# Kernel optimization log

Measured on AMD Instinct MI355X. Metric: run time of the kernel, lower is better.

The kernel has to match this reference:

```python
import math
import jax, jax.numpy as jnp
import numpy as np

B, L, D = 2, 2048, 768
H, DK = 12, 64
NUM_BUCKETS, MAX_DIST = 32, 128


def _relative_position_bucket(rel, bidirectional=True, num_buckets=32, max_distance=128):
    # rel: [Lq, Lk] int32, rel = k_pos - q_pos
    ret = jnp.zeros_like(rel)
    n = -rel
    if bidirectional:
        num_buckets //= 2
        ret = ret + (n < 0).astype(jnp.int32) * num_buckets
        n = jnp.abs(n)
    else:
        n = jnp.maximum(n, 0)
    max_exact = num_buckets // 2
    is_small = n < max_exact
    # safe log: avoid log(0); masked by where(is_small, ...)
    n_safe = jnp.maximum(n, 1).astype(jnp.float32)
    val_if_large = max_exact + (
        jnp.log(n_safe / max_exact) / math.log(max_distance / max_exact) * (num_buckets - max_exact)
    ).astype(jnp.int32)
    val_if_large = jnp.minimum(val_if_large, num_buckets - 1)
    return ret + jnp.where(is_small, n, val_if_large)


def setup_inputs() -> dict:
    key = jax.random.key(0)
    ks = jax.random.split(key, 7)
    s = 1.0 / math.sqrt(D)
    return {
        "query": jax.random.normal(ks[0], (B, L, D), jnp.float32),
        "key_value": jax.random.normal(ks[1], (B, L, D), jnp.float32),
        "key_padding_mask": jnp.ones((B, L), jnp.int32),
        "Wq": jax.random.normal(ks[2], (D, H * DK), jnp.float32) * s,
        "Wk": jax.random.normal(ks[3], (D, H * DK), jnp.float32) * s,
        "Wv": jax.random.normal(ks[4], (D, H * DK), jnp.float32) * s,
        "Wo": jax.random.normal(ks[5], (H * DK, D), jnp.float32) * s,
        "rel_emb": jax.random.normal(ks[6], (NUM_BUCKETS, H), jnp.float32),
    }


def reference(query, key_value, key_padding_mask, Wq, Wk, Wv, Wo, rel_emb):
    Bq, Lq, _ = query.shape
    Lk = key_value.shape[1]
    scale = DK ** (-0.5)

    Q = (query @ Wq).reshape(Bq, Lq, H, DK).transpose(0, 2, 1, 3)      # [B,H,Lq,DK]
    K = (key_value @ Wk).reshape(Bq, Lk, H, DK).transpose(0, 2, 1, 3)  # [B,H,Lk,DK]
    V = (key_value @ Wv).reshape(Bq, Lk, H, DK).transpose(0, 2, 1, 3)

    scores = jnp.einsum("bhqd,bhkd->bhqk", Q, K) * scale               # [B,H,Lq,Lk]

    # T5 relative position bias (bidirectional, causal_mask=False)
    rel = jnp.arange(Lk, dtype=jnp.int32)[None, :] - jnp.arange(Lq, dtype=jnp.int32)[:, None]
    buckets = _relative_position_bucket(rel, True, NUM_BUCKETS, MAX_DIST)  # [Lq,Lk]
    bias = rel_emb[buckets]                                             # [Lq,Lk,H]
    scores = scores + bias.transpose(2, 0, 1)[None]                     # [1,H,Lq,Lk]

    pad = (key_padding_mask == 0)[:, None, None, :]                     # [B,1,1,Lk]
    scores = jnp.where(pad, -jnp.inf, scores)

    attn = jax.nn.softmax(scores.astype(jnp.float32), axis=-1).astype(Q.dtype)
    out = jnp.einsum("bhqk,bhkd->bhqd", attn, V)                        # [B,H,Lq,DK]
    out = out.transpose(0, 2, 1, 3).reshape(Bq, Lq, H * DK)
    return out @ Wo
```

## Files before the change

kernel.cpp:

```cpp
#include <hip/hip_runtime.h>
#include <stdint.h>

typedef __attribute__((ext_vector_type(8))) short bf16x8;
typedef __attribute__((ext_vector_type(4))) float f32x4;
typedef __attribute__((ext_vector_type(4))) unsigned int u32x4;

#define NB 2
#define NL 2048
#define ND 768
#define NH 12
#define NDK 64
#define NM 4096
#define LOG2E 1.4426950408889634f

template<int N> struct IC { static constexpr int v = N; };

__device__ __forceinline__ unsigned short f2bf(float f) {
  unsigned u = __builtin_bit_cast(unsigned, f);
  u += 0x7FFFu + ((u >> 16) & 1u);
  return (unsigned short)(u >> 16);
}

__device__ __forceinline__ float fexp2(float x) {
  float r;
  asm("v_exp_f32 %0, %1" : "=v"(r) : "v"(x));
  return r;
}

__device__ __forceinline__ float xmax32(float x) { return fmaxf(x, __shfl_xor(x, 32)); }
__device__ __forceinline__ float xsum32(float x) { return x + __shfl_xor(x, 32); }

__device__ __forceinline__ void gl_lds16(const unsigned short* g, unsigned short* l) {
  __builtin_amdgcn_global_load_lds((const __attribute__((address_space(1))) void*)g,
                                   (__attribute__((address_space(3))) void*)l, 16, 0, 0);
}

__global__ __launch_bounds__(256) void k_prep(const float* __restrict__ query,
                                              const float* __restrict__ keyval,
                                              const float* __restrict__ Wq,
                                              const float* __restrict__ Wk,
                                              const float* __restrict__ Wv,
                                              const float* __restrict__ Wo,
                                              const float* __restrict__ rel_emb,
                                              const int* __restrict__ mask,
                                              unsigned short* __restrict__ q_bf,
                                              unsigned short* __restrict__ kv_bf,
                                              unsigned short* __restrict__ Wq_t,
                                              unsigned short* __restrict__ Wk_t,
                                              unsigned short* __restrict__ Wv_t,
                                              unsigned short* __restrict__ Wo_t,
                                              float* __restrict__ bias_tab,
                                              float* __restrict__ maskadd,
                                              int* __restrict__ maskall) {
  __shared__ float shbuf[32 * 33];
  int blk = blockIdx.x, tid = threadIdx.x;
  if (blk < 6144) {
    int y = blk / 3072;
    int i = (blk - y * 3072) * 256 + tid;
    const float* src = y ? keyval : query;
    unsigned short* dst = y ? kv_bf : q_bf;
    float4 v = ((const float4*)src)[i];
    ushort4 o;
    o.x = f2bf(v.x); o.y = f2bf(v.y); o.z = f2bf(v.z); o.w = f2bf(v.w);
    ((ushort4*)dst)[i] = o;
  } else if (blk < 8448) {
    int rel = blk - 6144;
    int z = rel / 576, r2 = rel - z * 576;
    int bx = (r2 % 24) * 32, by = (r2 / 24) * 32;
    const float* w = (z == 0) ? Wq : (z == 1) ? Wk : (z == 2) ? Wv : Wo;
    unsigned short* o = (z == 0) ? Wq_t : (z == 1) ? Wk_t : (z == 2) ? Wv_t : Wo_t;
    float scale = (z == 0) ? 0.125f * LOG2E : 1.0f;
    int tx = tid & 31, ty = tid >> 5;
    float (*t)[33] = (float(*)[33])shbuf;
    for (int r = 0; r < 32; r += 8)
      t[ty + r][tx] = w[(by + ty + r) * ND + bx + tx];
    __syncthreads();
    for (int r = 0; r < 32; r += 8)
      o[(bx + ty + r) * ND + by + tx] = f2bf(t[tx][ty + r] * scale);
  } else if (blk < 8640) {
    int idx = (blk - 8448) * 256 + tid;
    if (idx >= 4095 * NH) return;
    int h = idx % NH;
    int di = idx / NH;
    int rel = di - 2047;
    int n = -rel;
    int ret = 0;
    if (n < 0) { ret = 16; n = -n; }
    int b;
    if (n < 8) {
      b = ret + n;
    } else {
      int v = (n >= 91) ? 7 : (n >= 64) ? 6 : (n >= 46) ? 5 : (n >= 32) ? 4
            : (n >= 23) ? 3 : (n >= 16) ? 2 : (n >= 12) ? 1 : 0;
      b = ret + 8 + v;
    }
    bias_tab[h * 4095 + di] = rel_emb[b * NH + h] * LOG2E;
  } else {
    int b = blk - 8640;
    int* red = (int*)shbuf;
    int acc = 1;
    for (int i = tid; i < NL; i += 256) {
      int m = mask[b * NL + i];
      maskadd[b * NL + i] = m ? 0.0f : -1e30f;
      acc &= (m != 0) ? 1 : 0;
    }
    red[tid] = acc;
    __syncthreads();
    for (int s2 = 128; s2 > 0; s2 >>= 1) {
      if (tid < s2) red[tid] &= red[tid + s2];
      __syncthreads();
    }
    if (tid == 0) maskall[b] = red[0];
  }
}

__global__ __launch_bounds__(256) void k_gemm_qkv(const unsigned short* __restrict__ q_bf,
                                                  const unsigned short* __restrict__ kv_bf,
                                                  const unsigned short* __restrict__ Wt,
                                                  unsigned short* __restrict__ Qb,
                                                  unsigned short* __restrict__ Kb,
                                                  unsigned short* __restrict__ Vt) {
  __shared__ unsigned short S[14336];
  unsigned short* As = S;
  unsigned short* Bs = S + 8192;
  int tid = threadIdx.x;
  int wave = tid >> 6, lane = tid & 63;
  int lr = lane & 15, lg = lane >> 4;
  int m0 = blockIdx.x * 128;
  int z = blockIdx.y >> 3;
  int nc0 = (blockIdx.y & 7) * 96;
  const unsigned short* A  = (z == 0) ? q_bf : kv_bf;
  const unsigned short* Bt = Wt + (size_t)blockIdx.y * 96 * ND;
  int wm = (wave >> 1) * 64, wn = (wave & 1) * 48;
  int srow = tid >> 3, spc = tid & 7;
  int sg = spc ^ (srow & 7);
  const unsigned short* Ag = A  + (size_t)(m0 + srow) * ND + sg * 8;
  const unsigned short* Bg = Bt + (size_t)srow * ND + sg * 8;
  f32x4 acc[4][3] = {};
  for (int t = 0; t < ND / 64; ++t) {
    int k0 = t * 64;
#pragma unroll
    for (int s = 0; s < 4; ++s)
      gl_lds16(Ag + (size_t)(s * 32) * ND + k0, &As[s * 2048 + tid * 8]);
#pragma unroll
    for (int s = 0; s < 3; ++s)
      gl_lds16(Bg + (size_t)(s * 32) * ND + k0, &Bs[s * 2048 + tid * 8]);
    __syncthreads();
#pragma unroll
    for (int ks = 0; ks < 2; ++ks) {
      bf16x8 af[4], bfr[3];
#pragma unroll
      for (int i = 0; i < 4; ++i) {
        int ar = wm + i * 16 + lr;
        af[i] = *(const bf16x8*)&As[ar * 64 + (((ks * 4 + lg) ^ (ar & 7)) * 8)];
      }
#pragma unroll
      for (int i = 0; i < 3; ++i) {
        int br = wn + i * 16 + lr;
        bfr[i] = *(const bf16x8*)&Bs[br * 64 + (((ks * 4 + lg) ^ (br & 7)) * 8)];
      }
#pragma unroll
      for (int mi = 0; mi < 4; ++mi)
#pragma unroll
        for (int ni = 0; ni < 3; ++ni)
          acc[mi][ni] = __builtin_amdgcn_mfma_f32_16x16x32_bf16(af[mi], bfr[ni], acc[mi][ni], 0, 0, 0);
    }
    __syncthreads();
  }
  if (z == 2) {
    unsigned short* T = S;
#pragma unroll
    for (int mi = 0; mi < 4; ++mi)
#pragma unroll
      for (int ni = 0; ni < 3; ++ni) {
        int col  = wn + ni * 16 + lr;
        int rowb = wm + mi * 16 + lg * 4;
        ushort4 v4;
        v4.x = f2bf(acc[mi][ni][0]);
        v4.y = f2bf(acc[mi][ni][1]);
        v4.z = f2bf(acc[mi][ni][2]);
        v4.w = f2bf(acc[mi][ni][3]);
        int addr = col * 128 + (((rowb >> 3) ^ (col & 7)) * 8) + (rowb & 7);
        *(ushort4*)&T[addr] = v4;
      }
    __syncthreads();
    int bb = m0 >> 11;
    unsigned short* vdst = Vt + (((size_t)bb * ND + nc0) << 11) + (m0 & 2047);
#pragma unroll
    for (int pass = 0; pass < 6; ++pass) {
      int col = (tid >> 4) + pass * 16;
      int cc = tid & 15;
      u32x4 val = *(const u32x4*)&T[col * 128 + ((cc ^ (col & 7)) * 8)];
      *(u32x4*)&vdst[((size_t)col << 11) + cc * 8] = val;
    }
  } else {
#pragma unroll
    for (int mi = 0; mi < 4; ++mi)
#pragma unroll
      for (int ni = 0; ni < 3; ++ni)
#pragma unroll
        for (int r = 0; r < 4; ++r) {
          int row = m0 + wm + mi * 16 + lg * 4 + r;
          int col = nc0 + wn + ni * 16 + lr;
          unsigned short v = f2bf(acc[mi][ni][r]);
          if (z == 0) Qb[(size_t)row * ND + col] = v;
          else        Kb[(size_t)row * ND + col] = v;
        }
  }
}

__global__ __launch_bounds__(256) void k_gemm(const unsigned short* __restrict__ A,
                                              const unsigned short* __restrict__ Bt,
                                              float* __restrict__ Cout,
                                              int Msz, int Nsz, int Ksz) {
  __shared__ unsigned short As[4096];
  __shared__ unsigned short Bs[4096];
  int tid = threadIdx.x;
  int wave = tid >> 6, lane = tid & 63;
  int lr = lane & 15, lg = lane >> 4;
  int m0 = blockIdx.x * 64, n0 = blockIdx.y * 64;
  int wm = (wave >> 1) * 32, wn = (wave & 1) * 32;
  int srow = tid >> 3, spc = tid & 7;
  int sg = spc ^ (srow & 7);
  const unsigned short* Ag = A  + (size_t)(m0 + srow) * Ksz + sg * 8;
  const unsigned short* Bg = Bt + (size_t)(n0 + srow) * Ksz + sg * 8;
  f32x4 acc[2][2] = {};
  for (int t = 0; t < Ksz / 64; ++t) {
    int k0 = t * 64;
#pragma unroll
    for (int s = 0; s < 2; ++s) {
      gl_lds16(Ag + (size_t)(s * 32) * Ksz + k0, &As[s * 2048 + tid * 8]);
      gl_lds16(Bg + (size_t)(s * 32) * Ksz + k0, &Bs[s * 2048 + tid * 8]);
    }
    __syncthreads();
#pragma unroll
    for (int ks = 0; ks < 2; ++ks) {
      bf16x8 af[2], bfr[2];
#pragma unroll
      for (int i = 0; i < 2; ++i) {
        int ar = wm + i * 16 + lr;
        af[i] = *(const bf16x8*)&As[ar * 64 + (((ks * 4 + lg) ^ (ar & 7)) * 8)];
        int br = wn + i * 16 + lr;
        bfr[i] = *(const bf16x8*)&Bs[br * 64 + (((ks * 4 + lg) ^ (br & 7)) * 8)];
      }
#pragma unroll
      for (int mi = 0; mi < 2; ++mi)
#pragma unroll
        for (int ni = 0; ni < 2; ++ni)
          acc[mi][ni] = __builtin_amdgcn_mfma_f32_16x16x32_bf16(af[mi], bfr[ni], acc[mi][ni], 0, 0, 0);
    }
    __syncthreads();
  }
#pragma unroll
  for (int mi = 0; mi < 2; ++mi)
#pragma unroll
    for (int ni = 0; ni < 2; ++ni)
#pragma unroll
      for (int r = 0; r < 4; ++r) {
        int row = m0 + wm + mi * 16 + lg * 4 + r;
        int col = n0 + wn + ni * 16 + lr;
        Cout[(size_t)row * Nsz + col] = acc[mi][ni][r];
      }
}

__global__ __launch_bounds__(256, 3) void k_attn(const unsigned short* __restrict__ Qb,
                                                 const unsigned short* __restrict__ Kb,
                                                 const unsigned short* __restrict__ Vt,
                                                 const float* __restrict__ bias_tab,
                                                 const float* __restrict__ maskadd,
                                                 const int* __restrict__ maskall,
                                                 unsigned short* __restrict__ Ob) {
  __shared__ unsigned short Ks[3][4096];
  __shared__ unsigned short Vs[3][4096];
  __shared__ float biasw[384];
  int flat = blockIdx.x;
  int nf = (flat & 7) * 96 + (flat >> 3);
  int qt = nf & 31, bh = nf >> 5;
  int b = bh / NH, h = bh % NH;
  int tid = threadIdx.x, wave = tid >> 6, lane = tid & 63;
  int lr = lane & 15, lg = lane >> 4;
  int q0 = qt * 64;
  for (int i = tid; i < 383; i += 256) biasw[i] = bias_tab[h * 4095 + 1856 + i];
  float cFlo = bias_tab[h * 4095];
  float cFhi = bias_tab[h * 4095 + 4094];
  const unsigned short* Kbase = Kb + (size_t)(b * NL) * ND + h * NDK;
  const unsigned short* Vbase = Vt + (size_t)(b * NH + h) * NDK * NL;
  int srow = tid >> 3, spc = tid & 7;
  int sg = spc ^ (srow & 7);
  int l0 = (srow >> 4) * 32 + ((srow >> 2) & 3) * 8 + (srow & 3);
  const unsigned short* Kg0 = Kbase + (size_t)l0 * ND + sg * 8;
  const unsigned short* Kg1 = Kbase + (size_t)(l0 + 4) * ND + sg * 8;
  const unsigned short* Vg0 = Vbase + (size_t)srow * NL + sg * 8;
  const unsigned short* Vg1 = Vbase + (size_t)(32 + srow) * NL + sg * 8;
  bf16x8 aq[2];
  int qw = q0 + wave * 16;
#pragma unroll
  for (int ks = 0; ks < 2; ++ks)
    aq[ks] = *(const bf16x8*)&Qb[(size_t)(b * NL + qw + lr) * ND + h * NDK + ks * 32 + lg * 8];
  const float* cbase = maskadd + b * NL;
  int nomask = __builtin_amdgcn_readfirstlane(maskall[b]);
  f32x4 accO[4] = {};
  float mst = -1e30f, lstl = 0.f;
  int bconst = lg * 8 - wave * 16 - lr + 191 - q0;
  int src0 = (lane & 48) | ((lane >> 2) & 12);
  gl_lds16(Kg0, &Ks[0][tid * 8]);
  gl_lds16(Kg1, &Ks[0][2048 + tid * 8]);
  gl_lds16(Vg0, &Vs[0][tid * 8]);
  gl_lds16(Vg1, &Vs[0][2048 + tid * 8]);
  {
    size_t kok = (size_t)64 * ND, kov = 64;
    gl_lds16(Kg0 + kok, &Ks[1][tid * 8]);
    gl_lds16(Kg1 + kok, &Ks[1][2048 + tid * 8]);
    gl_lds16(Vg0 + kov, &Vs[1][tid * 8]);
    gl_lds16(Vg1 + kov, &Vs[1][2048 + tid * 8]);
  }
  asm volatile("s_waitcnt vmcnt(4) lgkmcnt(0)" ::: "memory");
  __builtin_amdgcn_s_barrier();
  const unsigned short* sk0 = Kg0 + (size_t)2 * 64 * ND;
  const unsigned short* sk1 = Kg1 + (size_t)2 * 64 * ND;
  const unsigned short* sv0 = Vg0 + 2 * 64;
  const unsigned short* sv1 = Vg1 + 2 * 64;

  auto body = [&](int kt_, auto CURc, auto PFc) {
    constexpr int CUR = decltype(CURc)::v;
    constexpr int PF  = decltype(PFc)::v;
    constexpr int ST  = (CUR + 2) % 3;
    float4 cv[2][2];
    if (!nomask) {
#pragma unroll
      for (int hf = 0; hf < 2; ++hf)
#pragma unroll
        for (int qd = 0; qd < 2; ++qd)
          cv[hf][qd] = *(const float4*)&cbase[kt_ * 64 + hf * 32 + lg * 8 + qd * 4];
    }
    if (PF) {
      gl_lds16(sk0, &Ks[ST][tid * 8]);
      gl_lds16(sk1, &Ks[ST][2048 + tid * 8]);
      gl_lds16(sv0, &Vs[ST][tid * 8]);
      gl_lds16(sv1, &Vs[ST][2048 + tid * 8]);
      sk0 += 64 * ND; sk1 += 64 * ND; sv0 += 64; sv1 += 64;
    }
    int kt64 = kt_ * 64;
    bool farlo = (kt64 + 63 < q0 - 90), farhi = (kt64 > q0 + 153);
    float ctile = farlo ? cFlo : (farhi ? cFhi : 0.0f);
    f32x4 s[4];
    __builtin_amdgcn_s_setprio(1);
    if (nomask && (farlo || farhi)) {
      const f32x4 z = {0.f, 0.f, 0.f, 0.f};
#pragma unroll
      for (int ni = 0; ni < 4; ++ni) {
        int kr = ni * 16 + lr;
        bf16x8 bk0 = *(const bf16x8*)&Ks[CUR][kr * 64 + ((lg ^ (lr & 7)) * 8)];
        bf16x8 bk1 = *(const bf16x8*)&Ks[CUR][kr * 64 + (((4 + lg) ^ (lr & 7)) * 8)];
        s[ni] = __builtin_amdgcn_mfma_f32_16x16x32_bf16(bk0, aq[0], z, 0, 0, 0);
        s[ni] = __builtin_amdgcn_mfma_f32_16x16x32_bf16(bk1, aq[1], s[ni], 0, 0, 0);
      }
    } else {
      if (farlo || farhi) {
#pragma unroll
        for (int ni = 0; ni < 4; ++ni)
#pragma unroll
          for (int r = 0; r < 4; ++r) s[ni][r] = 0.f;
      } else {
#pragma unroll
        for (int ni = 0; ni < 4; ++ni)
#pragma unroll
          for (int r = 0; r < 4; ++r)
            s[ni][r] = biasw[kt64 + (ni & 1) * 32 + (ni >> 1) * 4 + r + bconst];
      }
      if (!nomask) {
#pragma unroll
        for (int ni = 0; ni < 4; ++ni)
#pragma unroll
          for (int r = 0; r < 4; ++r)
            s[ni][r] += ((const float*)&cv[ni & 1][ni >> 1])[r];
      }
#pragma unroll
      for (int ni = 0; ni < 4; ++ni) {
        int kr = ni * 16 + lr;
        bf16x8 bk0 = *(const bf16x8*)&Ks[CUR][kr * 64 + ((lg ^ (lr & 7)) * 8)];
        bf16x8 bk1 = *(const bf16x8*)&Ks[CUR][kr * 64 + (((4 + lg) ^ (lr & 7)) * 8)];
        s[ni] = __builtin_amdgcn_mfma_f32_16x16x32_bf16(bk0, aq[0], s[ni], 0, 0, 0);
        s[ni] = __builtin_amdgcn_mfma_f32_16x16x32_bf16(bk1, aq[1], s[ni], 0, 0, 0);
      }
    }
    __builtin_amdgcn_s_setprio(0);
    f32x4 t0, t1;
#pragma unroll
    for (int r = 0; r < 4; ++r) t0[r] = fmaxf(s[0][r], s[1][r]);
#pragma unroll
    for (int r = 0; r < 4; ++r) t1[r] = fmaxf(s[2][r], s[3][r]);
#pragma unroll
    for (int r = 0; r < 4; ++r) t0[r] = fmaxf(t0[r], t1[r]);
    float lm = fmaxf(fmaxf(t0[0], t0[1]), fmaxf(t0[2], t0[3]));
    if (!__all(lm + ctile - mst <= 8.0f)) {
      float pmax = fmaxf(lm, __shfl_xor(lm, 16));
      pmax = xmax32(pmax);
      float pm2 = pmax + ctile;
      float mnew = fmaxf(mst, pm2);
      float sc = fexp2(mst - mnew);
      float scB[4];
#pragma unroll
      for (int r = 0; r < 4; ++r) scB[r] = __shfl(sc, src0 | r);
#pragma unroll
      for (int ni = 0; ni < 4; ++ni)
#pragma unroll
        for (int r = 0; r < 4; ++r) accO[ni][r] *= scB[r];
      lstl *= sc;
      mst = mnew;
    }
    float msub = mst - ctile;
#pragma unroll
    for (int ni = 0; ni < 4; ++ni)
#pragma unroll
      for (int r = 0; r < 4; ++r) s[ni][r] = fexp2(s[ni][r] - msub);
    {
      f32x4 ta = s[0] + s[1];
      f32x4 tb = s[2] + s[3];
      ta = ta + tb;
      lstl += (ta[0] + ta[1]) + (ta[2] + ta[3]);
    }
    unsigned pw[8];
#pragma unroll
    for (int ni = 0; ni < 4; ++ni) {
      unsigned a, c;
      asm("v_cvt_pk_bf16_f32 %0, %1, %2" : "=v"(a) : "v"(s[ni][0]), "v"(s[ni][1]));
      asm("v_cvt_pk_bf16_f32 %0, %1, %2" : "=v"(c) : "v"(s[ni][2]), "v"(s[ni][3]));
      pw[ni * 2] = a; pw[ni * 2 + 1] = c;
    }
    u32x4 apw0 = {pw[0], pw[1], pw[4], pw[5]};
    u32x4 apw1 = {pw[2], pw[3], pw[6], pw[7]};
    bf16x8 ap0 = __builtin_bit_cast(bf16x8, apw0);
    bf16x8 ap1 = __builtin_bit_cast(bf16x8, apw1);
    __builtin_amdgcn_s_setprio(1);
#pragma unroll
    for (int ni = 0; ni < 4; ++ni) {
      int vr = ni * 16 + lr;
      bf16x8 bv0 = *(const bf16x8*)&Vs[CUR][vr * 64 + ((lg ^ (lr & 7)) * 8)];
      bf16x8 bv1 = *(const bf16x8*)&Vs[CUR][vr * 64 + (((4 + lg) ^ (lr & 7)) * 8)];
      accO[ni] = __builtin_amdgcn_mfma_f32_16x16x32_bf16(ap0, bv0, accO[ni], 0, 0, 0);
      accO[ni] = __builtin_amdgcn_mfma_f32_16x16x32_bf16(ap1, bv1, accO[ni], 0, 0, 0);
    }
    __builtin_amdgcn_s_setprio(0);
    if (PF) asm volatile("s_waitcnt vmcnt(4)" ::: "memory");
    else    asm volatile("s_waitcnt vmcnt(0)" ::: "memory");
    __builtin_amdgcn_s_barrier();
  };

  for (int kt = 0; kt < 30; kt += 3) {
    body(kt,     IC<0>{}, IC<1>{});
    body(kt + 1, IC<1>{}, IC<1>{});
    body(kt + 2, IC<2>{}, IC<1>{});
  }
  body(30, IC<0>{}, IC<0>{});
  body(31, IC<1>{}, IC<0>{});

  float lst = lstl + __shfl_xor(lstl, 16);
  lst = xsum32(lst);
  float linv = 1.0f / lst;
  float lB[4];
#pragma unroll
  for (int r = 0; r < 4; ++r) lB[r] = __shfl(linv, src0 | r);
#pragma unroll
  for (int ni = 0; ni < 4; ++ni)
#pragma unroll
    for (int r = 0; r < 4; ++r) {
      int qg = qw + lg * 4 + r;
      int col = h * NDK + ni * 16 + lr;
      Ob[(size_t)(b * NL + qg) * ND + col] = f2bf(accO[ni][r] * lB[r]);
    }
}

extern "C" void kernel_launch(void* const* d_in, const int* in_sizes, int n_in,
                              void* d_out, int out_size, void* d_ws, size_t ws_size,
                              hipStream_t stream) {
  const float* query  = (const float*)d_in[0];
  const float* keyval = (const float*)d_in[1];
  const int*   mask   = (const int*)d_in[2];
  const float* Wq     = (const float*)d_in[3];
  const float* Wk     = (const float*)d_in[4];
  const float* Wv     = (const float*)d_in[5];
  const float* Wo     = (const float*)d_in[6];
  const float* rel    = (const float*)d_in[7];

  char* ws = (char*)d_ws;
  unsigned short* q_bf  = (unsigned short*)(ws);
  unsigned short* kv_bf = (unsigned short*)(ws + 6291456);
  unsigned short* Wq_t  = (unsigned short*)(ws + 12582912);
  unsigned short* Wk_t  = (unsigned short*)(ws + 13762560);
  unsigned short* Wv_t  = (unsigned short*)(ws + 14942208);
  unsigned short* Wo_t  = (unsigned short*)(ws + 16121856);
  unsigned short* Qb    = (unsigned short*)(ws + 17301504);
  unsigned short* Kb    = (unsigned short*)(ws + 23592960);
  unsigned short* Vt    = (unsigned short*)(ws + 29884416);
  unsigned short* Ob    = (unsigned short*)(ws + 36175872);
  float* bias_tab       = (float*)(ws + 42467328);
  float* maskadd        = (float*)(ws + 42663936);
  int*   maskall        = (int*)(ws + 42680320);

  k_prep<<<dim3(8642), dim3(256), 0, stream>>>(query, keyval, Wq, Wk, Wv, Wo, rel, mask,
                                               q_bf, kv_bf, Wq_t, Wk_t, Wv_t, Wo_t,
                                               bias_tab, maskadd, maskall);
  k_gemm_qkv<<<dim3(32, 24), dim3(256), 0, stream>>>(q_bf, kv_bf, Wq_t, Qb, Kb, Vt);
  k_attn<<<dim3(768), dim3(256), 0, stream>>>(Qb, Kb, Vt, bias_tab, maskadd, maskall, Ob);
  k_gemm<<<dim3(64, 12), dim3(256), 0, stream>>>(Ob, Wo_t, (float*)d_out, NM, ND, ND);
}
```

Baseline: 93.31 us.

## Remap GEMM block indices for XCD locality and double-buffer output projection

Result: no change. 93.18 us (-0.1%).

```diff
diff --git a/kernel.cpp b/kernel.cpp
--- a/kernel.cpp
+++ b/kernel.cpp
@@ -123,14 +123,18 @@
   __shared__ unsigned short S[14336];
   unsigned short* As = S;
   unsigned short* Bs = S + 8192;
+  int flat = blockIdx.x;
+  int nf = (flat & 7) * 96 + (flat >> 3);
+  int px = nf / 24;
+  int y  = nf - px * 24;
   int tid = threadIdx.x;
   int wave = tid >> 6, lane = tid & 63;
   int lr = lane & 15, lg = lane >> 4;
-  int m0 = blockIdx.x * 128;
-  int z = blockIdx.y >> 3;
-  int nc0 = (blockIdx.y & 7) * 96;
+  int m0 = px * 128;
+  int z = y >> 3;
+  int nc0 = (y & 7) * 96;
   const unsigned short* A  = (z == 0) ? q_bf : kv_bf;
-  const unsigned short* Bt = Wt + (size_t)blockIdx.y * 96 * ND;
+  const unsigned short* Bt = Wt + (size_t)y * 96 * ND;
   int wm = (wave >> 1) * 64, wn = (wave & 1) * 48;
   int srow = tid >> 3, spc = tid & 7;
   int sg = spc ^ (srow & 7);
@@ -213,35 +217,48 @@
                                               const unsigned short* __restrict__ Bt,
                                               float* __restrict__ Cout,
                                               int Msz, int Nsz, int Ksz) {
-  __shared__ unsigned short As[4096];
-  __shared__ unsigned short Bs[4096];
+  __shared__ unsigned short As[2][4096];
+  __shared__ unsigned short Bs[2][4096];
+  int flat = blockIdx.x;
+  int nf = (flat & 7) * 96 + (flat >> 3);
+  int px = nf / 12;
+  int y  = nf - px * 12;
   int tid = threadIdx.x;
   int wave = tid >> 6, lane = tid & 63;
   int lr = lane & 15, lg = lane >> 4;
-  int m0 = blockIdx.x * 64, n0 = blockIdx.y * 64;
+  int m0 = px * 64, n0 = y * 64;
   int wm = (wave >> 1) * 32, wn = (wave & 1) * 32;
   int srow = tid >> 3, spc = tid & 7;
   int sg = spc ^ (srow & 7);
   const unsigned short* Ag = A  + (size_t)(m0 + srow) * Ksz + sg * 8;
   const unsigned short* Bg = Bt + (size_t)(n0 + srow) * Ksz + sg * 8;
   f32x4 acc[2][2] = {};
-  for (int t = 0; t < Ksz / 64; ++t) {
-    int k0 = t * 64;
-#pragma unroll
-    for (int s = 0; s < 2; ++s) {
-      gl_lds16(Ag + (size_t)(s * 32) * Ksz + k0, &As[s * 2048 + tid * 8]);
-      gl_lds16(Bg + (size_t)(s * 32) * Ksz + k0, &Bs[s * 2048 + tid * 8]);
-    }
-    __syncthreads();
+  const int KT = Ksz >> 6;
+#pragma unroll
+  for (int s = 0; s < 2; ++s) {
+    gl_lds16(Ag + (size_t)(s * 32) * Ksz, &As[0][s * 2048 + tid * 8]);
+    gl_lds16(Bg + (size_t)(s * 32) * Ksz, &Bs[0][s * 2048 + tid * 8]);
+  }
+  __syncthreads();
+  int cur = 0;
+  for (int t = 0; t < KT; ++t) {
+    if (t + 1 < KT) {
+      int k0 = (t + 1) << 6;
+#pragma unroll
+      for (int s = 0; s < 2; ++s) {
+        gl_lds16(Ag + (size_t)(s * 32) * Ksz + k0, &As[cur ^ 1][s * 2048 + tid * 8]);
+        gl_lds16(Bg + (size_t)(s * 32) * Ksz + k0, &Bs[cur ^ 1][s * 2048 + tid * 8]);
+      }
+    }
 #pragma unroll
     for (int ks = 0; ks < 2; ++ks) {
       bf16x8 af[2], bfr[2];
 #pragma unroll
       for (int i = 0; i < 2; ++i) {
         int ar = wm + i * 16 + lr;
-        af[i] = *(const bf16x8*)&As[ar * 64 + (((ks * 4 + lg) ^ (ar & 7)) * 8)];
+        af[i] = *(const bf16x8*)&As[cur][ar * 64 + (((ks * 4 + lg) ^ (ar & 7)) * 8)];
         int br = wn + i * 16 + lr;
-        bfr[i] = *(const bf16x8*)&Bs[br * 64 + (((ks * 4 + lg) ^ (br & 7)) * 8)];
+        bfr[i] = *(const bf16x8*)&Bs[cur][br * 64 + (((ks * 4 + lg) ^ (br & 7)) * 8)];
       }
 #pragma unroll
       for (int mi = 0; mi < 2; ++mi)
@@ -250,6 +267,7 @@
           acc[mi][ni] = __builtin_amdgcn_mfma_f32_16x16x32_bf16(af[mi], bfr[ni], acc[mi][ni], 0, 0, 0);
     }
     __syncthreads();
+    cur ^= 1;
   }
 #pragma unroll
   for (int mi = 0; mi < 2; ++mi)
@@ -501,7 +519,7 @@
   k_prep<<<dim3(8642), dim3(256), 0, stream>>>(query, keyval, Wq, Wk, Wv, Wo, rel, mask,
                                                q_bf, kv_bf, Wq_t, Wk_t, Wv_t, Wo_t,
                                                bias_tab, maskadd, maskall);
-  k_gemm_qkv<<<dim3(32, 24), dim3(256), 0, stream>>>(q_bf, kv_bf, Wq_t, Qb, Kb, Vt);
+  k_gemm_qkv<<<dim3(768), dim3(256), 0, stream>>>(q_bf, kv_bf, Wq_t, Qb, Kb, Vt);
   k_attn<<<dim3(768), dim3(256), 0, stream>>>(Qb, Kb, Vt, bias_tab, maskadd, maskall, Ob);
-  k_gemm<<<dim3(64, 12), dim3(256), 0, stream>>>(Ob, Wo_t, (float*)d_out, NM, ND, ND);
-}
+  k_gemm<<<dim3(768), dim3(256), 0, stream>>>(Ob, Wo_t, (float*)d_out, NM, ND, ND);
+}
```
